# Kernel tuning notes

Hardware: AMD Instinct MI355X
Metric: run time of the kernel (lower is better)

Reference implementation:

```python
import jax, jax.numpy as jnp
import numpy as np

SEQ_LEN, BATCH, INPUT_SIZE, HIDDEN = 2048, 512, 1, 25


def setup_inputs() -> dict:
    key = jax.random.key(0)
    ks = jax.random.split(key, 7)
    s = 1.0 / np.sqrt(HIDDEN)  # PyTorch LSTM init scale (uniform(-s, s)); use scaled normal for simplicity
    return {
        "x": jax.random.normal(ks[0], (SEQ_LEN, BATCH, INPUT_SIZE), dtype=jnp.float32),
        "W_ih": jax.random.normal(ks[1], (4 * HIDDEN, INPUT_SIZE), dtype=jnp.float32) * s,
        "W_hh": jax.random.normal(ks[2], (4 * HIDDEN, HIDDEN), dtype=jnp.float32) * s,
        "b_ih": jax.random.normal(ks[3], (4 * HIDDEN,), dtype=jnp.float32) * s,
        "b_hh": jax.random.normal(ks[4], (4 * HIDDEN,), dtype=jnp.float32) * s,
        "W_lin": jax.random.normal(ks[5], (1, HIDDEN), dtype=jnp.float32) * s,
        "b_lin": jax.random.normal(ks[6], (1,), dtype=jnp.float32) * s,
    }


def reference(x, W_ih, W_hh, b_ih, b_hh, W_lin, b_lin):
    # x: [T, B, input_size]; PyTorch gate order: i, f, g, o
    T, B, _ = x.shape
    H = W_hh.shape[1]
    b = b_ih + b_hh  # [4H]

    def step(carry, xt):
        h, c = carry                                  # [B, H] each
        gates = xt @ W_ih.T + h @ W_hh.T + b          # [B, 4H]
        i, f, g, o = jnp.split(gates, 4, axis=-1)
        i = jax.nn.sigmoid(i)
        f = jax.nn.sigmoid(f)
        g = jnp.tanh(g)
        o = jax.nn.sigmoid(o)
        c_new = f * c + i * g
        h_new = o * jnp.tanh(c_new)
        return (h_new, c_new), h_new

    h0 = jnp.zeros((B, H), dtype=x.dtype)
    c0 = jnp.zeros((B, H), dtype=x.dtype)
    _, hs = jax.lax.scan(step, (h0, c0), x)           # hs: [T, B, H]
    pred = hs @ W_lin.T + b_lin                        # [T, B, output_size]
    return pred
```

## Files before the change

### kernel.cpp

```cpp
#include <hip/hip_runtime.h>

#define SEQ_LEN 2048
#define BATCH   512
#define HIDDEN  25

typedef int v2i __attribute__((ext_vector_type(2)));
typedef _Float16 h2_t __attribute__((ext_vector_type(2)));

__device__ __forceinline__ float fast_rcp(float v)  { return __builtin_amdgcn_rcpf(v); }
__device__ __forceinline__ float fast_exp2(float v) { return __builtin_amdgcn_exp2f(v); }

__device__ __forceinline__ float fdot2i(int a, int b, float c) {
#if __has_builtin(__builtin_amdgcn_fdot2)
    return __builtin_amdgcn_fdot2(__builtin_bit_cast(h2_t, a), __builtin_bit_cast(h2_t, b), c, false);
#else
    float d;
    asm("v_dot2_f32_f16 %0, %1, %2, %3" : "=v"(d) : "v"(a), "v"(b), "v"(c));
    return d;
#endif
}

__device__ __forceinline__ float xswap32(float v) {
#if __has_builtin(__builtin_amdgcn_permlane32_swap)
    v2i r = __builtin_amdgcn_permlane32_swap(__float_as_int(v), __float_as_int(v), false, false);
    return (__int_as_float(r.x) + __int_as_float(r.y)) - v;
#else
    return __shfl_xor(v, 32);
#endif
}

__global__ __launch_bounds__(64)
__attribute__((amdgpu_waves_per_eu(1, 1)))
void lstm_kernel(
    const float* __restrict__ x,
    const float* __restrict__ W_ih,
    const float* __restrict__ W_hh,
    const float* __restrict__ b_ih,
    const float* __restrict__ b_hh,
    const float* __restrict__ W_lin,
    const float* __restrict__ b_lin,
    float* __restrict__ out)
{
    const int lane = threadIdx.x;
    const int b    = blockIdx.x;

    __shared__ float pp[64][29];

    const bool U  = (lane >= 32);
    const int  j  = lane & 31;
    const int  jj = (j < HIDDEN) ? j : 0;
    const bool hv = (j < HIDDEN);

    const int r1 = U ? (HIDDEN + jj) : jj;
    const int r2 = U ? (3 * HIDDEN + jj) : (2 * HIDDEN + jj);

    const float LOG2E = 1.4426950408889634f;
    const float s1 = -LOG2E;
    const float s2 = U ? -LOG2E : (-2.0f * LOG2E);

    float w1[26], w2[26];
    #pragma unroll
    for (int k = 0; k < HIDDEN; ++k) {
        w1[k] = W_hh[r1 * HIDDEN + k] * s1;
        w2[k] = W_hh[r2 * HIDDEN + k] * s2;
    }
    w1[25] = 0.0f; w2[25] = 0.0f;
    int W1p[13], W2p[13];
    #pragma unroll
    for (int m = 0; m < 13; ++m) {
        W1p[m] = __builtin_bit_cast(int, __builtin_amdgcn_cvt_pkrtz(w1[2*m], w1[2*m+1]));
        W2p[m] = __builtin_bit_cast(int, __builtin_amdgcn_cvt_pkrtz(w2[2*m], w2[2*m+1]));
    }
    float bias1 = (b_ih[r1] + b_hh[r1]) * s1;
    float bias2 = (b_ih[r2] + b_hh[r2]) * s2;
    float wi1   = W_ih[r1] * s1;
    float wi2   = W_ih[r2] * s2;

    #pragma unroll
    for (int m = 0; m < 13; ++m) {
        asm volatile("" : "+v"(W1p[m]));
        asm volatile("" : "+v"(W2p[m]));
    }
    asm volatile("" : "+v"(bias1), "+v"(bias2), "+v"(wi1), "+v"(wi2));

    const float wlin  = (U && hv) ? W_lin[jj] : 0.0f;
    const float blin  = b_lin[0];
    const int   pcol  = (U && hv) ? jj : 26;

    float cs = 0.0f;
    float vh = 0.0f;

    const float* xb = x + b;
    float xv = xb[(size_t)lane * BATCH];

    #pragma unroll 1
    for (int tb = 0; tb < SEQ_LEN; tb += 64) {
        float xv_next = 0.0f;
        if (tb + 64 < SEQ_LEN) xv_next = xb[(size_t)(tb + 64 + lane) * BATCH];

        #pragma unroll 4
        for (int tt = 0; tt < 64; ++tt) {
            const int vhn = __builtin_amdgcn_mov_dpp(__float_as_int(vh), 0xB1, 0xF, 0xF, true);
            const int hpk = __builtin_bit_cast(int,
                __builtin_amdgcn_cvt_pkrtz(vh, __int_as_float(vhn)));

            int hw[13];
            #pragma unroll
            for (int m = 0; m < 13; ++m)
                hw[m] = __builtin_amdgcn_readlane(hpk, 32 + 2 * m);

            const float xt = __int_as_float(__builtin_amdgcn_readlane(__float_as_int(xv), tt));

            float a1 = fmaf(xt, wi1, bias1);
            float a2 = fmaf(xt, wi2, bias2);
            float b1 = 0.0f, b2 = 0.0f;
            #pragma unroll
            for (int m = 0; m < 12; m += 2) {
                a1 = fdot2i(W1p[m],     hw[m],     a1);
                b1 = fdot2i(W1p[m + 1], hw[m + 1], b1);
                a2 = fdot2i(W2p[m],     hw[m],     a2);
                b2 = fdot2i(W2p[m + 1], hw[m + 1], b2);
            }
            a1 = fdot2i(W1p[12], hw[12], a1) + b1;
            a2 = fdot2i(W2p[12], hw[12], a2) + b2;

            const float R1 = fast_rcp(1.0f + fast_exp2(a1));
            const float R2 = fast_rcp(1.0f + fast_exp2(a2));

            const float Gp  = fmaf(R2, -4.0f * LOG2E, 2.0f * LOG2E);
            const float igs = R1 * Gp;
            const float igx = xswap32(igs);

            cs = fmaf(R1, cs, igx);
            const float R3 = fast_rcp(1.0f + fast_exp2(cs));
            const float o2 = R2 + R2;
            vh = fmaf(o2, R3, -R2);

            pp[tt][pcol] = vh * wlin;
        }
        __syncthreads();

        float s = blin;
        #pragma unroll
        for (int k = 0; k < HIDDEN; ++k) s += pp[lane][k];
        out[(size_t)(tb + lane) * BATCH + b] = s;
        __syncthreads();

        xv = xv_next;
    }
}

extern "C" void kernel_launch(void* const* d_in, const int* in_sizes, int n_in,
                              void* d_out, int out_size, void* d_ws, size_t ws_size,
                              hipStream_t stream) {
    const float* x     = (const float*)d_in[0];
    const float* W_ih  = (const float*)d_in[1];
    const float* W_hh  = (const float*)d_in[2];
    const float* b_ih  = (const float*)d_in[3];
    const float* b_hh  = (const float*)d_in[4];
    const float* W_lin = (const float*)d_in[5];
    const float* b_lin = (const float*)d_in[6];
    float* outp = (float*)d_out;

    hipLaunchKernelGGL(lstm_kernel, dim3(BATCH), dim3(64), 0, stream,
                       x, W_ih, W_hh, b_ih, b_hh, W_lin, b_lin, outp);
}
```

Measured before the change: 326.8 us.

## Interleave four independent batch chains per wavefront for ILP

Each single-wave block now handles four batch elements, interleaving their independent recurrences within one time step so that latency of dot/transcendental/cross-lane ops overlaps across chains. The grid shrinks from 512 to 128 blocks, leaving many CUs idle on a 256-CU device, and it also drops the inner-loop unroll and adds register pressure. This trades parallel occupancy for per-wave instruction-level parallelism.

```diff
diff --git a/kernel.cpp b/kernel.cpp
--- a/kernel.cpp
+++ b/kernel.cpp
@@ -3,6 +3,7 @@
 #define SEQ_LEN 2048
 #define BATCH   512
 #define HIDDEN  25
+#define NC      4
 
 typedef int v2i __attribute__((ext_vector_type(2)));
 typedef _Float16 h2_t __attribute__((ext_vector_type(2)));
@@ -42,9 +43,9 @@
     float* __restrict__ out)
 {
     const int lane = threadIdx.x;
-    const int b    = blockIdx.x;
+    const int bb   = blockIdx.x * NC;
 
-    __shared__ float pp[64][29];
+    __shared__ float pp[NC][64][29];
 
     const bool U  = (lane >= 32);
     const int  j  = lane & 31;
@@ -87,66 +88,89 @@
     const float blin  = b_lin[0];
     const int   pcol  = (U && hv) ? jj : 26;
 
-    float cs = 0.0f;
-    float vh = 0.0f;
+    float cs[NC], vh[NC], xv[NC], xvn[NC];
+    #pragma unroll
+    for (int c = 0; c < NC; ++c) { cs[c] = 0.0f; vh[c] = 0.0f; }
 
-    const float* xb = x + b;
-    float xv = xb[(size_t)lane * BATCH];
+    #pragma unroll
+    for (int c = 0; c < NC; ++c)
+        xv[c] = x[(size_t)lane * BATCH + bb + c];
 
     #pragma unroll 1
     for (int tb = 0; tb < SEQ_LEN; tb += 64) {
-        float xv_next = 0.0f;
-        if (tb + 64 < SEQ_LEN) xv_next = xb[(size_t)(tb + 64 + lane) * BATCH];
+        #pragma unroll
+        for (int c = 0; c < NC; ++c)
+            xvn[c] = (tb + 64 < SEQ_LEN) ? x[(size_t)(tb + 64 + lane) * BATCH + bb + c] : 0.0f;
 
-        #pragma unroll 4
+        #pragma unroll 1
         for (int tt = 0; tt < 64; ++tt) {
-            const int vhn = __builtin_amdgcn_mov_dpp(__float_as_int(vh), 0xB1, 0xF, 0xF, true);
-            const int hpk = __builtin_bit_cast(int,
-                __builtin_amdgcn_cvt_pkrtz(vh, __int_as_float(vhn)));
+            int hpk[NC];
+            #pragma unroll
+            for (int c = 0; c < NC; ++c) {
+                const int vhn = __builtin_amdgcn_mov_dpp(__float_as_int(vh[c]), 0xB1, 0xF, 0xF, true);
+                hpk[c] = __builtin_bit_cast(int,
+                    __builtin_amdgcn_cvt_pkrtz(vh[c], __int_as_float(vhn)));
+            }
 
-            int hw[13];
+            int hw[NC][13];
             #pragma unroll
-            for (int m = 0; m < 13; ++m)
-                hw[m] = __builtin_amdgcn_readlane(hpk, 32 + 2 * m);
+            for (int c = 0; c < NC; ++c)
+                #pragma unroll
+                for (int m = 0; m < 13; ++m)
+                    hw[c][m] = __builtin_amdgcn_readlane(hpk[c], 32 + 2 * m);
 
-            const float xt = __int_as_float(__builtin_amdgcn_readlane(__float_as_int(xv), tt));
+            float a1[NC], a2[NC];
+            #pragma unroll
+            for (int c = 0; c < NC; ++c) {
+                const float xt = __int_as_float(__builtin_amdgcn_readlane(__float_as_int(xv[c]), tt));
+                a1[c] = fmaf(xt, wi1, bias1);
+                a2[c] = fmaf(xt, wi2, bias2);
+            }
 
-            float a1 = fmaf(xt, wi1, bias1);
-            float a2 = fmaf(xt, wi2, bias2);
-            float b1 = 0.0f, b2 = 0.0f;
             #pragma unroll
-            for (int m = 0; m < 12; m += 2) {
-                a1 = fdot2i(W1p[m],     hw[m],     a1);
-                b1 = fdot2i(W1p[m + 1], hw[m + 1], b1);
-                a2 = fdot2i(W2p[m],     hw[m],     a2);
-                b2 = fdot2i(W2p[m + 1], hw[m + 1], b2);
+            for (int c = 0; c < NC; ++c) {
+                float b1 = 0.0f, b2 = 0.0f;
+                #pragma unroll
+                for (int m = 0; m < 12; m += 2) {
+                    a1[c] = fdot2i(W1p[m],     hw[c][m],     a1[c]);
+                    b1    = fdot2i(W1p[m + 1], hw[c][m + 1], b1);
+                    a2[c] = fdot2i(W2p[m],     hw[c][m],     a2[c]);
+                    b2    = fdot2i(W2p[m + 1], hw[c][m + 1], b2);
+                }
+                a1[c] = fdot2i(W1p[12], hw[c][12], a1[c]) + b1;
+                a2[c] = fdot2i(W2p[12], hw[c][12], a2[c]) + b2;
             }
-            a1 = fdot2i(W1p[12], hw[12], a1) + b1;
-            a2 = fdot2i(W2p[12], hw[12], a2) + b2;
 
-            const float R1 = fast_rcp(1.0f + fast_exp2(a1));
-            const float R2 = fast_rcp(1.0f + fast_exp2(a2));
+            #pragma unroll
+            for (int c = 0; c < NC; ++c) {
+                const float R1 = fast_rcp(1.0f + fast_exp2(a1[c]));
+                const float R2 = fast_rcp(1.0f + fast_exp2(a2[c]));
 
-            const float Gp  = fmaf(R2, -4.0f * LOG2E, 2.0f * LOG2E);
-            const float igs = R1 * Gp;
-            const float igx = xswap32(igs);
+                const float Gp  = fmaf(R2, -4.0f * LOG2E, 2.0f * LOG2E);
+                const float igs = R1 * Gp;
+                const float igx = xswap32(igs);
 
-            cs = fmaf(R1, cs, igx);
-            const float R3 = fast_rcp(1.0f + fast_exp2(cs));
-            const float o2 = R2 + R2;
-            vh = fmaf(o2, R3, -R2);
+                cs[c] = fmaf(R1, cs[c], igx);
+                const float R3 = fast_rcp(1.0f + fast_exp2(cs[c]));
+                const float o2 = R2 + R2;
+                vh[c] = fmaf(o2, R3, -R2);
 
-            pp[tt][pcol] = vh * wlin;
+                pp[c][tt][pcol] = vh[c] * wlin;
+            }
         }
         __syncthreads();
 
-        float s = blin;
         #pragma unroll
-        for (int k = 0; k < HIDDEN; ++k) s += pp[lane][k];
-        out[(size_t)(tb + lane) * BATCH + b] = s;
+        for (int c = 0; c < NC; ++c) {
+            float s = blin;
+            #pragma unroll
+            for (int k = 0; k < HIDDEN; ++k) s += pp[c][lane][k];
+            out[(size_t)(tb + lane) * BATCH + bb + c] = s;
+        }
         __syncthreads();
 
-        xv = xv_next;
+        #pragma unroll
+        for (int c = 0; c < NC; ++c) xv[c] = xvn[c];
     }
 }
 
@@ -162,6 +186,6 @@
     const float* b_lin = (const float*)d_in[6];
     float* outp = (float*)d_out;
 
-    hipLaunchKernelGGL(lstm_kernel, dim3(BATCH), dim3(64), 0, stream,
+    hipLaunchKernelGGL(lstm_kernel, dim3(BATCH / NC), dim3(64), 0, stream,
                        x, W_ih, W_hh, b_ih, b_hh, W_lin, b_lin, outp);
 }
```

Result: slower. 1.124 ms (+244.1%).
